# Kernel optimization log

Hardware: AMD Instinct MI355X
Metric: run time of the kernel (lower is better)

## Reference

```python
import jax, jax.numpy as jnp
import numpy as np
from jax import lax

C = 64
EPS = 1e-5


def _layernorm_c(x, g, b):
    # LayerNorm over channel dim of NCHW tensor (matches nn.LayerNorm([C]) applied on NHWC)
    mu = jnp.mean(x, axis=1, keepdims=True)
    var = jnp.var(x, axis=1, keepdims=True)
    xn = (x - mu) * lax.rsqrt(var + EPS)
    return xn * g[None, :, None, None] + b[None, :, None, None]


def _conv1x1(x, w, b):
    # w: [O, I]
    return jnp.einsum('bihw,oi->bohw', x, w) + b[None, :, None, None]


def _dwconv3x3(x, w, b):
    # depthwise 3x3, w: [C, 3, 3]
    k = w[:, None, :, :]  # OIHW with I=1
    y = lax.conv_general_dilated(x, k, (1, 1), 'SAME',
                                 feature_group_count=w.shape[0],
                                 dimension_numbers=('NCHW', 'OIHW', 'NCHW'))
    return y + b[None, :, None, None]


def setup_inputs() -> dict:
    key = jax.random.key(0)
    ks = jax.random.split(key, 24)
    s = 0.02
    d = {}
    d['x'] = jax.random.normal(ks[0], (4, C, 64, 64), dtype=jnp.float32)
    # CTA params
    d['cta_ln_g'] = jnp.ones((C,), jnp.float32)
    d['cta_ln_b'] = jnp.zeros((C,), jnp.float32)
    d['q_w'] = jax.random.normal(ks[1], (C, C), jnp.float32) * s
    d['q_b'] = jnp.zeros((C,), jnp.float32)
    d['k_w'] = jax.random.normal(ks[2], (C, 3, 3), jnp.float32) * s
    d['k_b'] = jnp.zeros((C,), jnp.float32)
    d['v_w'] = jax.random.normal(ks[3], (C, 3, 3), jnp.float32) * s
    d['v_b'] = jnp.zeros((C,), jnp.float32)
    d['cta_out_w'] = jax.random.normal(ks[4], (C, C), jnp.float32) * s
    d['cta_out_b'] = jnp.zeros((C,), jnp.float32)
    # NLE params
    d['nle_ln_g'] = jnp.ones((C,), jnp.float32)
    d['nle_ln_b'] = jnp.zeros((C,), jnp.float32)
    d['b1_w1'] = jax.random.normal(ks[5], (2 * C, C), jnp.float32) * s
    d['b1_b1'] = jnp.zeros((2 * C,), jnp.float32)
    d['b1_w2'] = jax.random.normal(ks[6], (2 * C, 3, 3), jnp.float32) * s
    d['b1_b2'] = jnp.zeros((2 * C,), jnp.float32)
    d['b2_w1'] = jax.random.normal(ks[7], (2 * C, C), jnp.float32) * s
    d['b2_b1'] = jnp.zeros((2 * C,), jnp.float32)
    d['b2_w2'] = jax.random.normal(ks[8], (2 * C, 3, 3), jnp.float32) * s
    d['b2_b2'] = jnp.zeros((2 * C,), jnp.float32)
    d['nle_out_w'] = jax.random.normal(ks[9], (C, 2 * C), jnp.float32) * s
    d['nle_out_b'] = jnp.zeros((C,), jnp.float32)
    return d


def csam_forward(x, cta_ln_g, cta_ln_b, q_w, q_b, k_w, k_b, v_w, v_b, cta_out_w, cta_out_b,
                 nle_ln_g, nle_ln_b, b1_w1, b1_b1, b1_w2, b1_b2, b2_w1, b2_b1, b2_w2, b2_b2,
                 nle_out_w, nle_out_b):
    B, Cc, H, W = x.shape
    scale = jnp.sqrt(jnp.float32(Cc))
    # --- CTA ---
    xn = _layernorm_c(x, cta_ln_g, cta_ln_b)
    q = _conv1x1(xn, q_w, q_b).reshape(B, Cc, H * W)      # [B,C,N]
    k = _dwconv3x3(xn, k_w, k_b).reshape(B, Cc, H * W)    # [B,C,N]
    v = _dwconv3x3(xn, v_w, v_b).reshape(B, Cc, H * W)    # [B,C,N]
    attn = jnp.einsum('bcn,bcm->bnm', q, k) / scale        # [B,N,N]
    attn = jax.nn.softmax(attn, axis=-1)
    out = jnp.einsum('bnm,bcm->bcn', attn, v).reshape(B, Cc, H, W)
    x_att = _conv1x1(out, cta_out_w, cta_out_b) + x
    # --- NLE ---
    xn2 = _layernorm_c(x_att, nle_ln_g, nle_ln_b)
    br1 = jax.nn.gelu(_dwconv3x3(_conv1x1(xn2, b1_w1, b1_b1), b1_w2, b1_b2), approximate=False)
    br2 = jax.nn.gelu(_dwconv3x3(_conv1x1(xn2, b2_w1, b2_b1), b2_w2, b2_b2), approximate=False)
    nle = _conv1x1(br1 * br2, nle_out_w, nle_out_b)
    return nle + x_att


def reference(x, cta_ln_g, cta_ln_b, q_w, q_b, k_w, k_b, v_w, v_b, cta_out_w, cta_out_b,
              nle_ln_g, nle_ln_b, b1_w1, b1_b1, b1_w2, b1_b2, b2_w1, b2_b1, b2_w2, b2_b2,
              nle_out_w, nle_out_b):
    return csam_forward(x, cta_ln_g, cta_ln_b, q_w, q_b, k_w, k_b, v_w, v_b, cta_out_w, cta_out_b,
                        nle_ln_g, nle_ln_b, b1_w1, b1_b1, b1_w2, b1_b2, b2_w1, b2_b1, b2_w2, b2_b2,
                        nle_out_w, nle_out_b)
```

## Files before the change

kernel.cpp:

```cpp
#include <hip/hip_runtime.h>
#include <hip/hip_bf16.h>
#include <math.h>

#define NPIX 4096
#define CH 64
#define BATCH 4
#define NSPLIT 4

typedef __attribute__((ext_vector_type(8))) short short8;
typedef __attribute__((ext_vector_type(4))) float f32x4;
typedef __attribute__((ext_vector_type(4))) unsigned short us4;
typedef __attribute__((ext_vector_type(4))) unsigned int u32x4;

static __device__ __forceinline__ unsigned short f2bf(float f) {
  union { float f; unsigned u; } v; v.f = f;
  unsigned u = v.u;
  unsigned r = u + 0x7FFF + ((u >> 16) & 1);
  return (unsigned short)(r >> 16);
}
static __device__ __forceinline__ float bf2f(unsigned short u) {
  union { unsigned u; float f; } v; v.u = ((unsigned)u) << 16; return v.f;
}

__global__ __launch_bounds__(256) void k_ln_q(
    const float* __restrict__ x, const float* __restrict__ lg, const float* __restrict__ lb,
    const float* __restrict__ qw, const float* __restrict__ qb,
    float* __restrict__ xn, unsigned short* __restrict__ Q)
{
  __shared__ float xT[64][64];
  __shared__ unsigned short xB[64][64];
  int tid = threadIdx.x, px = tid & 63, g4 = tid >> 6;
  int idx0 = blockIdx.x * 64;
  int idx = idx0 + px;
  int b = idx >> 12, p = idx & 4095;
  const float* xb = x + (size_t)b * CH * NPIX + p;
  for (int j = 0; j < 16; ++j) { int c = 16 * g4 + j; xT[c][px] = xb[(size_t)c * NPIX]; }
  __syncthreads();
  float xv[64]; float s = 0.f;
#pragma unroll
  for (int c = 0; c < 64; ++c) { xv[c] = xT[c][px]; s += xv[c]; }
  float mu = s * (1.f / 64.f), vs = 0.f;
#pragma unroll
  for (int c = 0; c < 64; ++c) { float d = xv[c] - mu; vs += d * d; }
  float rs = rsqrtf(vs * (1.f / 64.f) + 1e-5f);
#pragma unroll
  for (int c = 0; c < 64; ++c) xv[c] = (xv[c] - mu) * rs * lg[c] + lb[c];

  float* xnb = xn + (size_t)b * CH * NPIX + p;
#define LNQ_WR(C0)                                                             \
  {                                                                            \
    unsigned short t[16];                                                      \
    _Pragma("unroll") for (int j = 0; j < 16; ++j) {                           \
      float v = xv[C0 + j];                                                    \
      xnb[(size_t)(C0 + j) * NPIX] = v;                                        \
      t[j] = f2bf(v);                                                          \
    }                                                                          \
    *(short8*)&xB[px][(((C0 / 8) + 0) ^ (px & 7)) * 8] = *(short8*)t;          \
    *(short8*)&xB[px][(((C0 / 8) + 1) ^ (px & 7)) * 8] = *(short8*)(t + 8);    \
  }
  if (g4 == 0) LNQ_WR(0)
  else if (g4 == 1) LNQ_WR(16)
  else if (g4 == 2) LNQ_WR(32)
  else LNQ_WR(48)
#undef LNQ_WR
  __syncthreads();

  int lane = tid & 63, l15 = lane & 15, gg = lane >> 4;
  short8 af[2];
#pragma unroll
  for (int kc = 0; kc < 2; ++kc) {
    const float* wp = qw + (size_t)(g4 * 16 + l15) * 64 + kc * 32 + 8 * gg;
    unsigned short t[8];
#pragma unroll
    for (int j = 0; j < 8; ++j) t[j] = f2bf(wp[j]);
    af[kc] = *(short8*)t;
  }
  float bv[4];
#pragma unroll
  for (int r = 0; r < 4; ++r) bv[r] = qb[g4 * 16 + 4 * gg + r];
#pragma unroll
  for (int ct = 0; ct < 4; ++ct) {
    f32x4 acc = {bv[0], bv[1], bv[2], bv[3]};
    int row = ct * 16 + l15;
    short8 bf0 = *(const short8*)&xB[row][((0 + gg) ^ (row & 7)) * 8];
    short8 bf1 = *(const short8*)&xB[row][((4 + gg) ^ (row & 7)) * 8];
    acc = __builtin_amdgcn_mfma_f32_16x16x32_bf16(af[0], bf0, acc, 0, 0, 0);
    acc = __builtin_amdgcn_mfma_f32_16x16x32_bf16(af[1], bf1, acc, 0, 0, 0);
    us4 v;
#pragma unroll
    for (int r = 0; r < 4; ++r) v[r] = f2bf(acc[r] * 0.125f);
    *(us4*)(Q + (size_t)(idx0 + row) * 64 + g4 * 16 + 4 * gg) = v;
  }
}

__global__ __launch_bounds__(256) void k_dwkv(
    const float* __restrict__ xn,
    const float* __restrict__ kw, const float* __restrict__ kb,
    const float* __restrict__ vw, const float* __restrict__ vb,
    unsigned short* __restrict__ K, unsigned short* __restrict__ VT)
{
  int idx = blockIdx.x * 256 + threadIdx.x;
  int b = idx >> 12, p = idx & 4095;
  int h = p >> 6, w = p & 63;
  int c0 = blockIdx.y * 8;
  size_t base = (size_t)b * CH * NPIX;
  unsigned short kq[8];
#pragma unroll
  for (int j = 0; j < 8; ++j) {
    int c = c0 + j;
    const float* xc = xn + base + (size_t)c * NPIX;
    float ka = kb[c], va = vb[c];
#pragma unroll
    for (int dy = -1; dy <= 1; ++dy) {
#pragma unroll
      for (int dx = -1; dx <= 1; ++dx) {
        int hh = h + dy, ww = w + dx;
        float xvv = (hh >= 0 && hh < 64 && ww >= 0 && ww < 64) ? xc[hh * 64 + ww] : 0.f;
        int t = (dy + 1) * 3 + (dx + 1);
        ka += kw[c * 9 + t] * xvv;
        va += vw[c * 9 + t] * xvv;
      }
    }
    kq[j] = f2bf(ka);
    VT[((size_t)b * CH + c) * NPIX + p] = f2bf(va);
  }
  *(short8*)(K + (size_t)idx * 64 + c0) = *(short8*)(kq);
}

__global__ __launch_bounds__(256, 4) void k_attn(
    const unsigned short* __restrict__ Q, const unsigned short* __restrict__ K,
    const unsigned short* __restrict__ VT, unsigned short* __restrict__ OPb,
    float* __restrict__ LS)
{
  __shared__ unsigned short kls[2][64][64];
  __shared__ unsigned short vls[2][64][64];
  __shared__ unsigned short plds[4][16][64];

  int tid = threadIdx.x;
  int wid = tid >> 6;
  int lane = tid & 63;
  int l15 = lane & 15, g = lane >> 4;
  int b = blockIdx.y;
  int split = blockIdx.z;
  int nbase = blockIdx.x * 64 + wid * 16;

  const unsigned short* Qb = Q + (size_t)b * NPIX * CH;
  const unsigned short* Kb = K + (size_t)b * NPIX * CH;
  const unsigned short* Vb = VT + (size_t)b * CH * NPIX;

  short8 qf0 = *(const short8*)(Qb + (size_t)(nbase + l15) * CH + 8 * g);
  short8 qf1 = *(const short8*)(Qb + (size_t)(nbase + l15) * CH + 32 + 8 * g);

  f32x4 oacc[4];
#pragma unroll
  for (int i = 0; i < 4; ++i) oacc[i] = (f32x4){0.f, 0.f, 0.f, 0.f};
  float lsum[4] = {0.f, 0.f, 0.f, 0.f};
  unsigned short* pwv = &plds[wid][0][0];

  int srow = tid >> 3, sch = tid & 7;
  int wa0 = srow * 64 + ((sch ^ (srow & 7)) * 8);
  int srow1 = srow + 32;
  int wa1 = srow1 * 64 + ((sch ^ (srow1 & 7)) * 8);
  const unsigned short* ksrc0 = Kb + (size_t)(split * 1024 + srow) * CH + sch * 8;
  const unsigned short* ksrc1 = Kb + (size_t)(split * 1024 + srow1) * CH + sch * 8;
  const unsigned short* vsrc0 = Vb + (size_t)srow * NPIX + split * 1024 + sch * 8;
  const unsigned short* vsrc1 = Vb + (size_t)srow1 * NPIX + split * 1024 + sch * 8;

  short8 kg0, kg1, vg0, vg1;
  kg0 = *(const short8*)(ksrc0);
  kg1 = *(const short8*)(ksrc1);
  vg0 = *(const short8*)(vsrc0);
  vg1 = *(const short8*)(vsrc1);
  *(short8*)(&kls[0][0][0] + wa0) = kg0;
  *(short8*)(&kls[0][0][0] + wa1) = kg1;
  *(short8*)(&vls[0][0][0] + wa0) = vg0;
  *(short8*)(&vls[0][0][0] + wa1) = vg1;
  __syncthreads();

  for (int t = 0; t < 16; ++t) {
    if (t < 15) {
      int ko = (t + 1) * 64;
      kg0 = *(const short8*)(ksrc0 + (size_t)ko * CH);
      kg1 = *(const short8*)(ksrc1 + (size_t)ko * CH);
      vg0 = *(const short8*)(vsrc0 + ko);
      vg1 = *(const short8*)(vsrc1 + ko);
    }

    const unsigned short* kb = &kls[t & 1][0][0];
    const unsigned short* vb = &vls[t & 1][0][0];

    f32x4 s[4];
#pragma unroll
    for (int cb = 0; cb < 4; ++cb) {
      int row = cb * 16 + l15;
      short8 kf0 = *(const short8*)(kb + row * 64 + (((0 + g) ^ (row & 7)) * 8));
      short8 kf1 = *(const short8*)(kb + row * 64 + (((4 + g) ^ (row & 7)) * 8));
      f32x4 acc = {0.f, 0.f, 0.f, 0.f};
      acc = __builtin_amdgcn_mfma_f32_16x16x32_bf16(qf0, kf0, acc, 0, 0, 0);
      acc = __builtin_amdgcn_mfma_f32_16x16x32_bf16(qf1, kf1, acc, 0, 0, 0);
      s[cb] = acc;
    }

#pragma unroll
    for (int cb = 0; cb < 4; ++cb) {
#pragma unroll
      for (int r = 0; r < 4; ++r) {
        float p = __expf(s[cb][r]);
        lsum[r] += p;
        int row = 4 * g + r;
        int key = cb * 16 + l15;
        pwv[row * 64 + (((key >> 3) ^ (row & 7)) * 8) + (key & 7)] = f2bf(p);
      }
    }
    short8 pf0 = *(const short8*)(pwv + l15 * 64 + (((0 + g) ^ (l15 & 7)) * 8));
    short8 pf1 = *(const short8*)(pwv + l15 * 64 + (((4 + g) ^ (l15 & 7)) * 8));

#pragma unroll
    for (int cs = 0; cs < 4; ++cs) {
      int row = cs * 16 + l15;
      short8 vf0 = *(const short8*)(vb + row * 64 + (((0 + g) ^ (row & 7)) * 8));
      short8 vf1 = *(const short8*)(vb + row * 64 + (((4 + g) ^ (row & 7)) * 8));
      oacc[cs] = __builtin_amdgcn_mfma_f32_16x16x32_bf16(pf0, vf0, oacc[cs], 0, 0, 0);
      oacc[cs] = __builtin_amdgcn_mfma_f32_16x16x32_bf16(pf1, vf1, oacc[cs], 0, 0, 0);
    }

    if (t < 15) {
      unsigned short* kw_ = &kls[(t + 1) & 1][0][0];
      unsigned short* vw_ = &vls[(t + 1) & 1][0][0];
      *(short8*)(kw_ + wa0) = kg0;
      *(short8*)(kw_ + wa1) = kg1;
      *(short8*)(vw_ + wa0) = vg0;
      *(short8*)(vw_ + wa1) = vg1;
    }
    __syncthreads();
  }

#pragma unroll
  for (int m = 1; m <= 8; m <<= 1) {
#pragma unroll
    for (int r = 0; r < 4; ++r) lsum[r] += __shfl_xor(lsum[r], m, 64);
  }

  size_t sb = ((size_t)split * BATCH + b) * NPIX;
  unsigned short* Ob = OPb + (sb + nbase) * CH;
#pragma unroll
  for (int r = 0; r < 4; ++r) {
    int n = 4 * g + r;
    Ob[n * CH +  0 + l15] = f2bf(oacc[0][r]);
    Ob[n * CH + 16 + l15] = f2bf(oacc[1][r]);
    Ob[n * CH + 32 + l15] = f2bf(oacc[2][r]);
    Ob[n * CH + 48 + l15] = f2bf(oacc[3][r]);
    if (l15 == 0) LS[sb + nbase + n] = lsum[r];
  }
}

__global__ __launch_bounds__(256) void k_reduce(
    const unsigned short* __restrict__ OPb, const float* __restrict__ LSv,
    unsigned short* __restrict__ AOT)
{
  int tid = threadIdx.x;
  size_t e0 = (size_t)blockIdx.x * 4096;
#pragma unroll
  for (int h = 0; h < 2; ++h) {
    int off = (h * 256 + tid) * 8;
    int pix = blockIdx.x * 64 + (off >> 6);
    float sv[8] = {0.f, 0.f, 0.f, 0.f, 0.f, 0.f, 0.f, 0.f};
    float ls = 0.f;
#pragma unroll
    for (int sp = 0; sp < NSPLIT; ++sp) {
      short8 a = *(const short8*)(OPb + (size_t)sp * BATCH * NPIX * 64 + e0 + off);
#pragma unroll
      for (int j = 0; j < 8; ++j) sv[j] += bf2f((unsigned short)a[j]);
      ls += LSv[(size_t)sp * BATCH * NPIX + pix];
    }
    float inv = 1.f / ls;
    unsigned short t[8];
#pragma unroll
    for (int j = 0; j < 8; ++j) t[j] = f2bf(sv[j] * inv);
    *(short8*)(AOT + e0 + off) = *(short8*)t;
  }
}

__global__ __launch_bounds__(256) void k_proj_ln2(
    const unsigned short* __restrict__ AOT, const float* __restrict__ x,
    const float* __restrict__ ow, const float* __restrict__ ob,
    const float* __restrict__ lg, const float* __restrict__ lb,
    float* __restrict__ xatt, unsigned short* __restrict__ xn2T)
{
  __shared__ float sm1[4][4][16], sm2[4][4][16];
  int tid = threadIdx.x;
  int wid = tid >> 6, lane = tid & 63;
  int l15 = lane & 15, g = lane >> 4;
  int b = blockIdx.y, pxb = blockIdx.x * 64;
  const unsigned short* In = AOT + ((size_t)b * NPIX + pxb) * 64;

  short8 af[2];
#pragma unroll
  for (int kc = 0; kc < 2; ++kc) {
    const float* wp = ow + (size_t)(wid * 16 + l15) * 64 + kc * 32 + 8 * g;
    unsigned short t[8];
#pragma unroll
    for (int j = 0; j < 8; ++j) t[j] = f2bf(wp[j]);
    af[kc] = *(short8*)t;
  }
  float bv[4], lgv[4], lbv[4];
#pragma unroll
  for (int r = 0; r < 4; ++r) {
    int o = wid * 16 + 4 * g + r;
    bv[r] = ob[o]; lgv[r] = lg[o]; lbv[r] = lb[o];
  }
  f32x4 acc[4];
#pragma unroll
  for (int ct = 0; ct < 4; ++ct) acc[ct] = (f32x4){bv[0], bv[1], bv[2], bv[3]};
#pragma unroll
  for (int ct = 0; ct < 4; ++ct) {
    short8 bf0 = *(const short8*)(In + (size_t)(ct * 16 + l15) * 64 + 8 * g);
    short8 bf1 = *(const short8*)(In + (size_t)(ct * 16 + l15) * 64 + 32 + 8 * g);
    acc[ct] = __builtin_amdgcn_mfma_f32_16x16x32_bf16(af[0], bf0, acc[ct], 0, 0, 0);
    acc[ct] = __builtin_amdgcn_mfma_f32_16x16x32_bf16(af[1], bf1, acc[ct], 0, 0, 0);
  }

  float xo[4][4];
#pragma unroll
  for (int ct = 0; ct < 4; ++ct) {
    int p = pxb + ct * 16 + l15;
    float s1 = 0.f, s2 = 0.f;
#pragma unroll
    for (int r = 0; r < 4; ++r) {
      int o = wid * 16 + 4 * g + r;
      size_t oi = ((size_t)b * CH + o) * NPIX + p;
      float v = acc[ct][r] + x[oi];
      xatt[oi] = v;
      xo[ct][r] = v;
      s1 += v; s2 += v * v;
    }
    s1 += __shfl_xor(s1, 16, 64); s1 += __shfl_xor(s1, 32, 64);
    s2 += __shfl_xor(s2, 16, 64); s2 += __shfl_xor(s2, 32, 64);
    if (g == 0) { sm1[wid][ct][l15] = s1; sm2[wid][ct][l15] = s2; }
  }
  __syncthreads();
#pragma unroll
  for (int ct = 0; ct < 4; ++ct) {
    int p = pxb + ct * 16 + l15;
    float mu = (sm1[0][ct][l15] + sm1[1][ct][l15] + sm1[2][ct][l15] + sm1[3][ct][l15]) * (1.f / 64.f);
    float ms = (sm2[0][ct][l15] + sm2[1][ct][l15] + sm2[2][ct][l15] + sm2[3][ct][l15]) * (1.f / 64.f);
    float rs = rsqrtf(ms - mu * mu + 1e-5f);
    us4 v4;
#pragma unroll
    for (int r = 0; r < 4; ++r) v4[r] = f2bf((xo[ct][r] - mu) * rs * lgv[r] + lbv[r]);
    *(us4*)(xn2T + ((size_t)b * NPIX + p) * 64 + wid * 16 + 4 * g) = v4;
  }
}

__global__ __launch_bounds__(256) void k_pw_both(
    const unsigned short* __restrict__ xn2T,
    const float* __restrict__ w1, const float* __restrict__ bb1,
    const float* __restrict__ w2, const float* __restrict__ bb2,
    float* __restrict__ t1, float* __restrict__ t2)
{
  int tid = threadIdx.x;
  int wid = tid >> 6, lane = tid & 63;
  int l15 = lane & 15, g = lane >> 4;
  int b = blockIdx.y, pxb = blockIdx.x * 64;
  const unsigned short* In = xn2T + ((size_t)b * NPIX + pxb) * 64;
  const float* W  = (wid & 2) ? w2 : w1;
  const float* bb = (wid & 2) ? bb2 : bb1;
  float* t        = (wid & 2) ? t2 : t1;
  int oh = (wid & 1) * 64;

  short8 af[4][2];
#pragma unroll
  for (int ot = 0; ot < 4; ++ot)
#pragma unroll
    for (int kc = 0; kc < 2; ++kc) {
      const float* wp = W + (size_t)(oh + ot * 16 + l15) * 64 + kc * 32 + 8 * g;
      unsigned short tt[8];
#pragma unroll
      for (int j = 0; j < 8; ++j) tt[j] = f2bf(wp[j]);
      af[ot][kc] = *(short8*)tt;
    }
  f32x4 acc[4][4];
#pragma unroll
  for (int ot = 0; ot < 4; ++ot) {
    float b0 = bb[oh + ot * 16 + 4 * g + 0];
    float b1 = bb[oh + ot * 16 + 4 * g + 1];
    float b2 = bb[oh + ot * 16 + 4 * g + 2];
    float b3 = bb[oh + ot * 16 + 4 * g + 3];
#pragma unroll
    for (int ct = 0; ct < 4; ++ct) acc[ot][ct] = (f32x4){b0, b1, b2, b3};
  }
#pragma unroll
  for (int ct = 0; ct < 4; ++ct) {
    short8 bf0 = *(const short8*)(In + (size_t)(ct * 16 + l15) * 64 + 8 * g);
    short8 bf1 = *(const short8*)(In + (size_t)(ct * 16 + l15) * 64 + 32 + 8 * g);
#pragma unroll
    for (int ot = 0; ot < 4; ++ot) {
      acc[ot][ct] = __builtin_amdgcn_mfma_f32_16x16x32_bf16(af[ot][0], bf0, acc[ot][ct], 0, 0, 0);
      acc[ot][ct] = __builtin_amdgcn_mfma_f32_16x16x32_bf16(af[ot][1], bf1, acc[ot][ct], 0, 0, 0);
    }
  }
#pragma unroll
  for (int ot = 0; ot < 4; ++ot)
#pragma unroll
    for (int ct = 0; ct < 4; ++ct) {
      int p = pxb + ct * 16 + l15;
#pragma unroll
      for (int r = 0; r < 4; ++r) {
        int o = oh + ot * 16 + 4 * g + r;
        t[((size_t)b * 128 + o) * NPIX + p] = acc[ot][ct][r];
      }
    }
}

__global__ __launch_bounds__(256) void k_dwgelu(
    const float* __restrict__ t1, const float* __restrict__ t2,
    const float* __restrict__ w1, const float* __restrict__ bb1,
    const float* __restrict__ w2, const float* __restrict__ bb2,
    unsigned short* __restrict__ g12T)
{
  int idx = blockIdx.x * 256 + threadIdx.x;
  int b = idx >> 12, p = idx & 4095;
  int h = p >> 6, w = p & 63;
  int c0 = blockIdx.y * 8;
  unsigned short outv[8];
#pragma unroll
  for (int j = 0; j < 8; ++j) {
    int c = c0 + j;
    size_t tb = ((size_t)b * 128 + c) * NPIX;
    float a1 = bb1[c], a2 = bb2[c];
#pragma unroll
    for (int dy = -1; dy <= 1; ++dy) {
#pragma unroll
      for (int dx = -1; dx <= 1; ++dx) {
        int hh = h + dy, ww = w + dx;
        bool ok = (hh >= 0 && hh < 64 && ww >= 0 && ww < 64);
        float v1 = ok ? t1[tb + hh * 64 + ww] : 0.f;
        float v2 = ok ? t2[tb + hh * 64 + ww] : 0.f;
        int t = (dy + 1) * 3 + (dx + 1);
        a1 += w1[c * 9 + t] * v1;
        a2 += w2[c * 9 + t] * v2;
      }
    }
    float ge1 = 0.5f * a1 * (1.f + erff(a1 * 0.70710678118654752f));
    float ge2 = 0.5f * a2 * (1.f + erff(a2 * 0.70710678118654752f));
    outv[j] = f2bf(ge1 * ge2);
  }
  *(short8*)(g12T + (size_t)idx * 128 + c0) = *(short8*)outv;
}

__global__ __launch_bounds__(256) void k_out(
    const float* __restrict__ W, const float* __restrict__ bias,
    const unsigned short* __restrict__ InT, const float* __restrict__ res,
    float* __restrict__ outF)
{
  int tid = threadIdx.x;
  int wid = tid >> 6, lane = tid & 63;
  int l15 = lane & 15, g = lane >> 4;
  int b = blockIdx.y, pxb = blockIdx.x * 64;
  const unsigned short* In = InT + ((size_t)b * NPIX + pxb) * 128;

  short8 af[4];
#pragma unroll
  for (int kc = 0; kc < 4; ++kc) {
    const float* wp = W + (size_t)(wid * 16 + l15) * 128 + kc * 32 + 8 * g;
    unsigned short t[8];
#pragma unroll
    for (int j = 0; j < 8; ++j) t[j] = f2bf(wp[j]);
    af[kc] = *(short8*)t;
  }
  float bv[4];
#pragma unroll
  for (int r = 0; r < 4; ++r) bv[r] = bias[wid * 16 + 4 * g + r];
#pragma unroll
  for (int ct = 0; ct < 4; ++ct) {
    f32x4 acc = {bv[0], bv[1], bv[2], bv[3]};
#pragma unroll
    for (int kc = 0; kc < 4; ++kc) {
      short8 bf = *(const short8*)(In + (size_t)(ct * 16 + l15) * 128 + kc * 32 + 8 * g);
      acc = __builtin_amdgcn_mfma_f32_16x16x32_bf16(af[kc], bf, acc, 0, 0, 0);
    }
    int p = pxb + ct * 16 + l15;
#pragma unroll
    for (int r = 0; r < 4; ++r) {
      int o = wid * 16 + 4 * g + r;
      size_t oi = ((size_t)b * CH + o) * NPIX + p;
      outF[oi] = acc[r] + res[oi];
    }
  }
}

extern "C" void kernel_launch(void* const* d_in, const int* in_sizes, int n_in,
                              void* d_out, int out_size, void* d_ws, size_t ws_size,
                              hipStream_t stream) {
  const float* x        = (const float*)d_in[0];
  const float* cta_ln_g = (const float*)d_in[1];
  const float* cta_ln_b = (const float*)d_in[2];
  const float* q_w      = (const float*)d_in[3];
  const float* q_b      = (const float*)d_in[4];
  const float* k_w      = (const float*)d_in[5];
  const float* k_b      = (const float*)d_in[6];
  const float* v_w      = (const float*)d_in[7];
  const float* v_b      = (const float*)d_in[8];
  const float* cta_out_w= (const float*)d_in[9];
  const float* cta_out_b= (const float*)d_in[10];
  const float* nle_ln_g = (const float*)d_in[11];
  const float* nle_ln_b = (const float*)d_in[12];
  const float* b1_w1    = (const float*)d_in[13];
  const float* b1_b1    = (const float*)d_in[14];
  const float* b1_w2    = (const float*)d_in[15];
  const float* b1_b2    = (const float*)d_in[16];
  const float* b2_w1    = (const float*)d_in[17];
  const float* b2_b1    = (const float*)d_in[18];
  const float* b2_w2    = (const float*)d_in[19];
  const float* b2_b2    = (const float*)d_in[20];
  const float* nle_out_w= (const float*)d_in[21];
  const float* nle_out_b= (const float*)d_in[22];

  char* ws = (char*)d_ws;
  float*          xn   = (float*)(ws);
  unsigned short* Qb   = (unsigned short*)(ws + (4u  << 20));
  unsigned short* Kb   = (unsigned short*)(ws + (6u  << 20));
  unsigned short* VTb  = (unsigned short*)(ws + (8u  << 20));
  unsigned short* OPb  = (unsigned short*)(ws + (10u << 20));
  float*          LSb  = (float*)(ws + (18u << 20));
  unsigned short* AOT  = (unsigned short*)(ws + (19u << 20));
  float*          xatt = (float*)(ws + (21u << 20));
  unsigned short* xn2T = (unsigned short*)(ws + (25u << 20));
  float*          t1   = (float*)(ws + (27u << 20));
  float*          t2   = (float*)(ws + (35u << 20));
  unsigned short* g12T = (unsigned short*)(ws);

  k_ln_q     <<<256, 256, 0, stream>>>(x, cta_ln_g, cta_ln_b, q_w, q_b, xn, Qb);
  k_dwkv     <<<dim3(64, 8), 256, 0, stream>>>(xn, k_w, k_b, v_w, v_b, Kb, VTb);
  k_attn     <<<dim3(64, BATCH, NSPLIT), 256, 0, stream>>>(Qb, Kb, VTb, OPb, LSb);
  k_reduce   <<<256, 256, 0, stream>>>(OPb, LSb, AOT);
  k_proj_ln2 <<<dim3(64, 4), 256, 0, stream>>>(AOT, x, cta_out_w, cta_out_b, nle_ln_g, nle_ln_b, xatt, xn2T);
  k_pw_both  <<<dim3(64, 4), 256, 0, stream>>>(xn2T, b1_w1, b1_b1, b2_w1, b2_b1, t1, t2);
  k_dwgelu   <<<dim3(64, 16), 256, 0, stream>>>(t1, t2, b1_w2, b1_b2, b2_w2, b2_b2, g12T);
  k_out      <<<dim3(64, 4), 256, 0, stream>>>(nle_out_w, nle_out_b, g12T, xatt, (float*)d_out);
}
```

Before: 80.53 us.

## Keep attention probabilities in registers via transposed MFMA and permuted key rows

Computes S^T = K·Q^T with a permuted key-row mapping, so each lane's exp'd scores land directly in the B-operand layout for the P·V MFMA. This removes the per-wave LDS staging buffer for P, its scattered stores and reloads, and the multi-step row-sum shuffle. The key/value LDS swizzle changes to a new XOR pattern to fit the new access shape, scores are packed with v_cvt_pk_bf16_f32, and output is written as vector stores. The risks are that the new permutation and swizzle must match exactly and that bank conflicts may change.

```diff
diff --git a/kernel.cpp b/kernel.cpp
--- a/kernel.cpp
+++ b/kernel.cpp
@@ -20,6 +20,11 @@
 }
 static __device__ __forceinline__ float bf2f(unsigned short u) {
   union { unsigned u; float f; } v; v.u = ((unsigned)u) << 16; return v.f;
+}
+static __device__ __forceinline__ unsigned cvtpk(float lo, float hi) {
+  unsigned r;
+  asm("v_cvt_pk_bf16_f32 %0, %1, %2" : "=v"(r) : "v"(lo), "v"(hi));
+  return r;
 }
 
 __global__ __launch_bounds__(256) void k_ln_q(
@@ -127,6 +132,7 @@
   *(short8*)(K + (size_t)idx * 64 + c0) = *(short8*)(kq);
 }
 
+#define SW(r) ((((r) & 7) ^ (((r) >> 3) << 1)) & 7)
 __global__ __launch_bounds__(256, 4) void k_attn(
     const unsigned short* __restrict__ Q, const unsigned short* __restrict__ K,
     const unsigned short* __restrict__ VT, unsigned short* __restrict__ OPb,
@@ -134,14 +140,11 @@
 {
   __shared__ unsigned short kls[2][64][64];
   __shared__ unsigned short vls[2][64][64];
-  __shared__ unsigned short plds[4][16][64];
 
   int tid = threadIdx.x;
-  int wid = tid >> 6;
-  int lane = tid & 63;
+  int wid = tid >> 6, lane = tid & 63;
   int l15 = lane & 15, g = lane >> 4;
-  int b = blockIdx.y;
-  int split = blockIdx.z;
+  int b = blockIdx.y, split = blockIdx.z;
   int nbase = blockIdx.x * 64 + wid * 16;
 
   const unsigned short* Qb = Q + (size_t)b * NPIX * CH;
@@ -151,20 +154,21 @@
   short8 qf0 = *(const short8*)(Qb + (size_t)(nbase + l15) * CH + 8 * g);
   short8 qf1 = *(const short8*)(Qb + (size_t)(nbase + l15) * CH + 32 + 8 * g);
 
-  f32x4 oacc[4];
-#pragma unroll
-  for (int i = 0; i < 4; ++i) oacc[i] = (f32x4){0.f, 0.f, 0.f, 0.f};
-  float lsum[4] = {0.f, 0.f, 0.f, 0.f};
-  unsigned short* pwv = &plds[wid][0][0];
+  f32x4 acc[4];
+#pragma unroll
+  for (int i = 0; i < 4; ++i) acc[i] = (f32x4){0.f, 0.f, 0.f, 0.f};
+  float lsum = 0.f;
 
   int srow = tid >> 3, sch = tid & 7;
-  int wa0 = srow * 64 + ((sch ^ (srow & 7)) * 8);
   int srow1 = srow + 32;
-  int wa1 = srow1 * 64 + ((sch ^ (srow1 & 7)) * 8);
+  int wa0 = srow * 64 + ((sch ^ SW(srow)) * 8);
+  int wa1 = srow1 * 64 + ((sch ^ SW(srow1)) * 8);
   const unsigned short* ksrc0 = Kb + (size_t)(split * 1024 + srow) * CH + sch * 8;
   const unsigned short* ksrc1 = Kb + (size_t)(split * 1024 + srow1) * CH + sch * 8;
   const unsigned short* vsrc0 = Vb + (size_t)srow * NPIX + split * 1024 + sch * 8;
   const unsigned short* vsrc1 = Vb + (size_t)srow1 * NPIX + split * 1024 + sch * 8;
+
+  int kperm = 8 * (l15 >> 2) + (l15 & 3);
 
   short8 kg0, kg1, vg0, vg1;
   kg0 = *(const short8*)(ksrc0);
@@ -189,39 +193,32 @@
     const unsigned short* kb = &kls[t & 1][0][0];
     const unsigned short* vb = &vls[t & 1][0][0];
 
-    f32x4 s[4];
-#pragma unroll
-    for (int cb = 0; cb < 4; ++cb) {
-      int row = cb * 16 + l15;
-      short8 kf0 = *(const short8*)(kb + row * 64 + (((0 + g) ^ (row & 7)) * 8));
-      short8 kf1 = *(const short8*)(kb + row * 64 + (((4 + g) ^ (row & 7)) * 8));
-      f32x4 acc = {0.f, 0.f, 0.f, 0.f};
-      acc = __builtin_amdgcn_mfma_f32_16x16x32_bf16(qf0, kf0, acc, 0, 0, 0);
-      acc = __builtin_amdgcn_mfma_f32_16x16x32_bf16(qf1, kf1, acc, 0, 0, 0);
-      s[cb] = acc;
-    }
-
-#pragma unroll
-    for (int cb = 0; cb < 4; ++cb) {
-#pragma unroll
-      for (int r = 0; r < 4; ++r) {
-        float p = __expf(s[cb][r]);
-        lsum[r] += p;
-        int row = 4 * g + r;
-        int key = cb * 16 + l15;
-        pwv[row * 64 + (((key >> 3) ^ (row & 7)) * 8) + (key & 7)] = f2bf(p);
+#pragma unroll
+    for (int s = 0; s < 2; ++s) {
+      int r0 = s * 32 + kperm;
+      int r1 = s * 32 + 4 + kperm;
+      short8 kf00 = *(const short8*)(kb + r0 * 64 + (((0 + g) ^ SW(r0)) * 8));
+      short8 kf01 = *(const short8*)(kb + r0 * 64 + (((4 + g) ^ SW(r0)) * 8));
+      short8 kf10 = *(const short8*)(kb + r1 * 64 + (((0 + g) ^ SW(r1)) * 8));
+      short8 kf11 = *(const short8*)(kb + r1 * 64 + (((4 + g) ^ SW(r1)) * 8));
+      f32x4 s0 = {0.f, 0.f, 0.f, 0.f}, s1 = {0.f, 0.f, 0.f, 0.f};
+      s0 = __builtin_amdgcn_mfma_f32_16x16x32_bf16(kf00, qf0, s0, 0, 0, 0);
+      s0 = __builtin_amdgcn_mfma_f32_16x16x32_bf16(kf01, qf1, s0, 0, 0, 0);
+      s1 = __builtin_amdgcn_mfma_f32_16x16x32_bf16(kf10, qf0, s1, 0, 0, 0);
+      s1 = __builtin_amdgcn_mfma_f32_16x16x32_bf16(kf11, qf1, s1, 0, 0, 0);
+      float p0 = __expf(s0[0]), p1 = __expf(s0[1]), p2 = __expf(s0[2]), p3 = __expf(s0[3]);
+      float p4 = __expf(s1[0]), p5 = __expf(s1[1]), p6 = __expf(s1[2]), p7 = __expf(s1[3]);
+      lsum += (p0 + p1) + (p2 + p3) + (p4 + p5) + (p6 + p7);
+      u32x4 pk;
+      pk[0] = cvtpk(p0, p1); pk[1] = cvtpk(p2, p3);
+      pk[2] = cvtpk(p4, p5); pk[3] = cvtpk(p6, p7);
+      short8 pb = *(short8*)&pk;
+#pragma unroll
+      for (int cs = 0; cs < 4; ++cs) {
+        int row = cs * 16 + l15;
+        short8 vf = *(const short8*)(vb + row * 64 + (((4 * s + g) ^ SW(row)) * 8));
+        acc[cs] = __builtin_amdgcn_mfma_f32_16x16x32_bf16(vf, pb, acc[cs], 0, 0, 0);
       }
-    }
-    short8 pf0 = *(const short8*)(pwv + l15 * 64 + (((0 + g) ^ (l15 & 7)) * 8));
-    short8 pf1 = *(const short8*)(pwv + l15 * 64 + (((4 + g) ^ (l15 & 7)) * 8));
-
-#pragma unroll
-    for (int cs = 0; cs < 4; ++cs) {
-      int row = cs * 16 + l15;
-      short8 vf0 = *(const short8*)(vb + row * 64 + (((0 + g) ^ (row & 7)) * 8));
-      short8 vf1 = *(const short8*)(vb + row * 64 + (((4 + g) ^ (row & 7)) * 8));
-      oacc[cs] = __builtin_amdgcn_mfma_f32_16x16x32_bf16(pf0, vf0, oacc[cs], 0, 0, 0);
-      oacc[cs] = __builtin_amdgcn_mfma_f32_16x16x32_bf16(pf1, vf1, oacc[cs], 0, 0, 0);
     }
 
     if (t < 15) {
@@ -235,24 +232,21 @@
     __syncthreads();
   }
 
-#pragma unroll
-  for (int m = 1; m <= 8; m <<= 1) {
-#pragma unroll
-    for (int r = 0; r < 4; ++r) lsum[r] += __shfl_xor(lsum[r], m, 64);
-  }
+  lsum += __shfl_xor(lsum, 16, 64);
+  lsum += __shfl_xor(lsum, 32, 64);
 
   size_t sb = ((size_t)split * BATCH + b) * NPIX;
-  unsigned short* Ob = OPb + (sb + nbase) * CH;
-#pragma unroll
-  for (int r = 0; r < 4; ++r) {
-    int n = 4 * g + r;
-    Ob[n * CH +  0 + l15] = f2bf(oacc[0][r]);
-    Ob[n * CH + 16 + l15] = f2bf(oacc[1][r]);
-    Ob[n * CH + 32 + l15] = f2bf(oacc[2][r]);
-    Ob[n * CH + 48 + l15] = f2bf(oacc[3][r]);
-    if (l15 == 0) LS[sb + nbase + n] = lsum[r];
-  }
-}
+  unsigned short* Ob = OPb + (sb + nbase + l15) * 64;
+#pragma unroll
+  for (int cs = 0; cs < 4; ++cs) {
+    us4 v;
+#pragma unroll
+    for (int r = 0; r < 4; ++r) v[r] = f2bf(acc[cs][r]);
+    *(us4*)(Ob + cs * 16 + 4 * g) = v;
+  }
+  if (g == 0) LS[sb + nbase + l15] = lsum;
+}
+#undef SW
 
 __global__ __launch_bounds__(256) void k_reduce(
     const unsigned short* __restrict__ OPb, const float* __restrict__ LSv,
```

Result: faster. 76.52 us (-5.0%).
